# Kernel optimization log

Measured on AMD Instinct MI355X. Metric: run time of the kernel, lower is better.

## Reference

```python
import jax, jax.numpy as jnp
import numpy as np

N_QUBITS = 8
N_LAYERS = 3
N_FEATURES = 16
BATCH = 65536
DIM = 2 ** N_QUBITS  # 256 amplitudes
EPS = 1e-5  # torch BatchNorm1d default eps

# Precompute CNOT permutations (wire 0 = most significant bit, PennyLane order)
_idx = np.arange(DIM)
CNOT_PERMS = []
for _i in range(N_QUBITS):
    for _j in range(_i + 1, N_QUBITS):
        _c = (_idx >> (N_QUBITS - 1 - _i)) & 1
        CNOT_PERMS.append(np.where(_c == 1, _idx ^ (1 << (N_QUBITS - 1 - _j)), _idx))
# PauliZ sign table: (DIM, N_QUBITS), +1 for bit 0, -1 for bit 1
Z_SIGNS = np.stack([1.0 - 2.0 * ((_idx >> (N_QUBITS - 1 - i)) & 1) for i in range(N_QUBITS)], axis=1).astype(np.float32)


def _ry(theta):
    t = jnp.asarray(theta)
    c = jnp.cos(t / 2).astype(jnp.complex64)
    s = jnp.sin(t / 2).astype(jnp.complex64)
    return jnp.stack([jnp.stack([c, -s], -1), jnp.stack([s, c], -1)], -2)


def _rx(theta):
    t = jnp.asarray(theta)
    c = jnp.cos(t / 2).astype(jnp.complex64)
    s = (-1j) * jnp.sin(t / 2).astype(jnp.complex64)
    return jnp.stack([jnp.stack([c, s], -1), jnp.stack([s, c], -1)], -2)


def _rz(theta):
    e = jnp.exp(-0.5j * jnp.asarray(theta, jnp.complex64))
    z = jnp.zeros_like(e)
    return jnp.stack([jnp.stack([e, z], -1), jnp.stack([z, jnp.conj(e)], -1)], -2)


def _apply_1q(state, U, w):
    # state: (B, DIM); U: (2,2) shared or (B,2,2) per-sample; wire w
    B = state.shape[0]
    left, right = 2 ** w, 2 ** (N_QUBITS - 1 - w)
    s = state.reshape(B, left, 2, right)
    if U.ndim == 2:
        out = jnp.einsum('st,bpsq->bptq', U, s)
    else:
        out = jnp.einsum('bst,bpsq->bptq', U, s)
    return out.reshape(B, DIM)


def _quantum(angles, qw):
    # Batched state-vector simulation of the PennyLane circuit.
    # angles: (B, N_QUBITS) float32 encoding angles; qw: (N_LAYERS, N_QUBITS, 3)
    B = angles.shape[0]
    state = jnp.zeros((B, DIM), jnp.complex64).at[:, 0].set(1.0 + 0.0j)
    for i in range(N_QUBITS):  # RY(inputs[i]) encoding, per-sample angles
        state = _apply_1q(state, _ry(angles[:, i]), i)
    for l in range(N_LAYERS):
        for i in range(N_QUBITS):
            state = _apply_1q(state, _rx(qw[l, i, 0]), i)
            state = _apply_1q(state, _ry(qw[l, i, 1]), i)
            state = _apply_1q(state, _rz(qw[l, i, 2]), i)
        for perm in CNOT_PERMS:  # all-pairs CNOT(i, j), i < j
            state = state[:, perm]
    probs = state.real ** 2 + state.imag ** 2  # (B, DIM)
    return probs @ jnp.asarray(Z_SIGNS)  # (B, N_QUBITS) <Z_i> expectations


def _bn(h, g, b, m, v):
    # BatchNorm1d in inference mode (running stats)
    return (h - m) * jax.lax.rsqrt(v + EPS) * g + b


def _forward(x, W1, b1, g1, bt1, m1, v1, W2, b2, g2, bt2, m2, v2, W3, b3, q_weights, W4, b4, g4, bt4, m4, v4, W5, b5, W6, b6):
    h = jax.nn.relu(_bn(x @ W1.T + b1, g1, bt1, m1, v1))
    h = jax.nn.relu(_bn(h @ W2.T + b2, g2, bt2, m2, v2))
    pre = jnp.tanh(h @ W3.T + b3)  # (B, N_QUBITS)
    # Original detaches before the quantum circuit -> no grad through it
    q_out = _quantum(jax.lax.stop_gradient(pre), jax.lax.stop_gradient(q_weights))
    h = jax.nn.relu(_bn(q_out @ W4.T + b4, g4, bt4, m4, v4))
    h = jax.nn.relu(h @ W5.T + b5)
    return h @ W6.T + b6  # (B, 1)


def setup_inputs() -> dict:
    key = jax.random.key(0)
    ks = jax.random.split(key, 8)

    def lin(k, o, i):
        return (jax.random.normal(k, (o, i), jnp.float32) / np.sqrt(i)).astype(jnp.float32)

    return {
        'x': jax.random.normal(ks[0], (BATCH, N_FEATURES), jnp.float32),
        'W1': lin(ks[1], 128, N_FEATURES), 'b1': jnp.zeros((128,), jnp.float32),
        'g1': jnp.ones((128,), jnp.float32), 'bt1': jnp.zeros((128,), jnp.float32),
        'm1': jnp.zeros((128,), jnp.float32), 'v1': jnp.ones((128,), jnp.float32),
        'W2': lin(ks[2], 64, 128), 'b2': jnp.zeros((64,), jnp.float32),
        'g2': jnp.ones((64,), jnp.float32), 'bt2': jnp.zeros((64,), jnp.float32),
        'm2': jnp.zeros((64,), jnp.float32), 'v2': jnp.ones((64,), jnp.float32),
        'W3': lin(ks[3], N_QUBITS, 64), 'b3': jnp.zeros((N_QUBITS,), jnp.float32),
        'q_weights': jax.random.normal(ks[4], (N_LAYERS, N_QUBITS, 3), jnp.float32) * 0.1,
        'W4': lin(ks[5], 32, N_QUBITS), 'b4': jnp.zeros((32,), jnp.float32),
        'g4': jnp.ones((32,), jnp.float32), 'bt4': jnp.zeros((32,), jnp.float32),
        'm4': jnp.zeros((32,), jnp.float32), 'v4': jnp.ones((32,), jnp.float32),
        'W5': lin(ks[6], 16, 32), 'b5': jnp.zeros((16,), jnp.float32),
        'W6': lin(ks[7], 1, 16), 'b6': jnp.zeros((1,), jnp.float32),
    }


def reference(x, W1, b1, g1, bt1, m1, v1, W2, b2, g2, bt2, m2, v2, W3, b3, q_weights, W4, b4, g4, bt4, m4, v4, W5, b5, W6, b6):
    return _forward(x, W1, b1, g1, bt1, m1, v1, W2, b2, g2, bt2, m2, v2, W3, b3, q_weights, W4, b4, g4, bt4, m4, v4, W5, b5, W6, b6)
```

## Files before the change

### kernel.cpp

```cpp
#include <hip/hip_runtime.h>

__device__ __forceinline__ float2 cmul(float2 a, float2 b){
    return make_float2(a.x*b.x - a.y*b.y, a.x*b.y + a.y*b.x);
}
__device__ __forceinline__ float2 cadd(float2 a, float2 b){
    return make_float2(a.x + b.x, a.y + b.y);
}
__device__ __forceinline__ unsigned short f2h(float f){
    _Float16 h = (_Float16)f;
    return __builtin_bit_cast(unsigned short, h);
}

typedef _Float16 f16x8 __attribute__((ext_vector_type(8)));
typedef float    f32x4 __attribute__((ext_vector_type(4)));

__device__ __forceinline__ void split8(const float* p, f16x8& ah, f16x8& al){
    const f32x4* q = (const f32x4*)p;
    f32x4 v0 = q[0], v1 = q[1];
    float av[8] = {v0[0],v0[1],v0[2],v0[3],v1[0],v1[1],v1[2],v1[3]};
    #pragma unroll
    for (int j=0;j<8;++j){
        _Float16 h = (_Float16)av[j];
        ah[j] = h;
        al[j] = (_Float16)(av[j] - (float)h);
    }
}

__device__ __forceinline__ void build_gates(const float* qw, int l, int c, float2 (*G)[2][2]){
    if (c < 8){
        int i = c;
        float t0 = 0.5f*qw[l*24 + i*3 + 0];
        float t1 = 0.5f*qw[l*24 + i*3 + 1];
        float t2 = 0.5f*qw[l*24 + i*3 + 2];
        float c1,s1,c2,s2,c3,s3;
        sincosf(t0,&s1,&c1); sincosf(t1,&s2,&c2); sincosf(t2,&s3,&c3);
        float2 RX[2][2] = {{{c1,0.f},{0.f,-s1}},{{0.f,-s1},{c1,0.f}}};
        float2 RY[2][2] = {{{c2,0.f},{s2,0.f}},{{-s2,0.f},{c2,0.f}}};
        float2 M[2][2];
        #pragma unroll
        for (int r=0;r<2;++r)
            #pragma unroll
            for (int cc=0;cc<2;++cc)
                M[r][cc] = cadd(cmul(RY[r][0],RX[0][cc]), cmul(RY[r][1],RX[1][cc]));
        float2 e  = {c3,-s3};
        float2 ec = {c3, s3};
        G[i][0][0]=cmul(e, M[0][0]); G[i][0][1]=cmul(e, M[0][1]);
        G[i][1][0]=cmul(ec,M[1][0]); G[i][1][1]=cmul(ec,M[1][1]);
    }
}
__device__ __forceinline__ int cnot_perm(int k){
    int r = k;
    for (int i=6;i>=0;--i)
        for (int j=7;j>i;--j)
            if ((r >> (7-i)) & 1) r ^= 1 << (7-j);
    return r;
}

__global__ void k_prep(const float* __restrict__ W1, const float* __restrict__ b1,
                       const float* __restrict__ g1, const float* __restrict__ bt1,
                       const float* __restrict__ m1, const float* __restrict__ v1,
                       const float* __restrict__ W2, const float* __restrict__ b2,
                       const float* __restrict__ g2, const float* __restrict__ bt2,
                       const float* __restrict__ m2, const float* __restrict__ v2,
                       const float* __restrict__ W3,
                       unsigned short* __restrict__ H1w, float* __restrict__ c1,
                       unsigned short* __restrict__ H2w, float* __restrict__ c2,
                       unsigned short* __restrict__ H3w){
    int tid = blockIdx.x*256 + threadIdx.x;
    int stride = gridDim.x*256;
    for (int i=tid; i<4096; i+=stride){ int n=i>>5, k=i&31;
        float s=g1[n]*rsqrtf(v1[n]+1e-5f);
        H1w[i] = f2h(k<16 ? W1[n*16+k]*s : 0.f); }
    for (int i=tid; i<128;  i+=stride){ float s=g1[i]*rsqrtf(v1[i]+1e-5f); c1[i]=(b1[i]-m1[i])*s+bt1[i]; }
    for (int i=tid; i<8192; i+=stride){ int n=i>>7;
        float s=g2[n]*rsqrtf(v2[n]+1e-5f);
        H2w[i] = f2h(W2[i]*s); }
    for (int i=tid; i<64;   i+=stride){ float s=g2[i]*rsqrtf(v2[i]+1e-5f); c2[i]=(b2[i]-m2[i])*s+bt2[i]; }
    for (int i=tid; i<1024; i+=stride){ int n=i>>6, k=i&63;
        H3w[i] = f2h(n<8 ? W3[n*64+k] : 0.f); }
}

__global__ void k_build_layers(const float* __restrict__ qw, float2* __restrict__ U){
    __shared__ float2 G[8][2][2];
    int l = blockIdx.y, k = blockIdx.x, c = threadIdx.x;
    build_gates(qw, l, c, G);
    __syncthreads();
    int r = cnot_perm(k);
    float2 p = {1.f, 0.f};
    #pragma unroll
    for (int i=0;i<8;++i)
        p = cmul(p, G[i][(r>>(7-i))&1][(c>>(7-i))&1]);
    U[l*65536 + k*256 + c] = p;
}

__global__ __launch_bounds__(256) void k_rowmm(const float* __restrict__ qw,
                                              const float2* __restrict__ U,
                                              unsigned short* __restrict__ W){
    __shared__ float2 G[8][2][2];
    __shared__ float2 vs[256];
    __shared__ float2 ws[256];
    int r = blockIdx.x, c = threadIdx.x;
    build_gates(qw, 2, c, G);
    __syncthreads();
    int pr = cnot_perm(r);
    float2 p = {1.f, 0.f};
    #pragma unroll
    for (int i=0;i<8;++i)
        p = cmul(p, G[i][(pr>>(7-i))&1][(c>>(7-i))&1]);
    vs[c] = p;
    __syncthreads();
    float2 acc = {0.f,0.f};
    #pragma unroll 8
    for (int m=0;m<256;++m)
        acc = cadd(acc, cmul(vs[m], U[65536 + m*256 + c]));
    ws[c] = acc;
    __syncthreads();
    float2 z = {0.f,0.f};
    #pragma unroll 8
    for (int m=0;m<256;++m)
        z = cadd(z, cmul(ws[m], U[m*256 + c]));
    W[r*256 + c]       = f2h(z.x);
    W[(r+256)*256 + c] = f2h(z.y);
}

__global__ __launch_bounds__(256,2) void k_front(
    const float* __restrict__ x,
    const unsigned short* __restrict__ H1w, const float* __restrict__ c1,
    const unsigned short* __restrict__ H2w, const float* __restrict__ c2,
    const unsigned short* __restrict__ H3w, const float* __restrict__ b3,
    float* __restrict__ pre)
{
    __shared__ __align__(16) char smem[60416];
    float* XS = (float*)smem;
    float* H1 = (float*)(smem + 9216);
    float* H2 = (float*)(smem + 43008);

    int tid = threadIdx.x;
    int row0 = blockIdx.x*64;
    {
        int r = tid >> 2, q = tid & 3;
        const float4* xp = (const float4*)(x + (row0 + r)*16 + q*4);
        float4 v = xp[0];
        *(float4*)(XS + r*36 + q*4) = v;
        *(float4*)(XS + r*36 + 16 + q*4) = make_float4(0.f,0.f,0.f,0.f);
    }
    __syncthreads();

    int wave = tid>>6, lane = tid&63, l15 = lane&15, lq = lane>>4;
    const f32x4 zz = {0.f,0.f,0.f,0.f};

    f32x4 acc1[4][2];
    #pragma unroll
    for (int mt=0;mt<4;++mt){ acc1[mt][0]=zz; acc1[mt][1]=zz; }
    #pragma unroll
    for (int mt=0; mt<4; ++mt){
        f16x8 ah, al;
        split8(XS + (mt*16+l15)*36 + lq*8, ah, al);
        #pragma unroll
        for (int t=0;t<2;++t){
            int nt = wave + t*4;
            f16x8 b = *(const f16x8*)(H1w + (nt*16+l15)*32 + lq*8);
            acc1[mt][t] = __builtin_amdgcn_mfma_f32_16x16x32_f16(ah, b, acc1[mt][t], 0,0,0);
            acc1[mt][t] = __builtin_amdgcn_mfma_f32_16x16x32_f16(al, b, acc1[mt][t], 0,0,0);
        }
    }
    #pragma unroll
    for (int t=0;t<2;++t){
        int n = (wave + t*4)*16 + l15;
        float bias = c1[n];
        #pragma unroll
        for (int mt=0; mt<4; ++mt)
            #pragma unroll
            for (int reg=0; reg<4; ++reg){
                int rowl = mt*16 + lq*4 + reg;
                H1[rowl*132 + n] = fmaxf(acc1[mt][t][reg] + bias, 0.f);
            }
    }
    __syncthreads();

    f32x4 acc2[4];
    #pragma unroll
    for (int mt=0;mt<4;++mt) acc2[mt]=zz;
    #pragma unroll
    for (int ks=0; ks<4; ++ks){
        f16x8 b = *(const f16x8*)(H2w + (wave*16+l15)*128 + ks*32 + lq*8);
        #pragma unroll
        for (int mt=0; mt<4; ++mt){
            f16x8 ah, al;
            split8(H1 + (mt*16+l15)*132 + ks*32 + lq*8, ah, al);
            acc2[mt] = __builtin_amdgcn_mfma_f32_16x16x32_f16(ah, b, acc2[mt], 0,0,0);
            acc2[mt] = __builtin_amdgcn_mfma_f32_16x16x32_f16(al, b, acc2[mt], 0,0,0);
        }
    }
    {
        int n = wave*16 + l15;
        float bias = c2[n];
        #pragma unroll
        for (int mt=0; mt<4; ++mt)
            #pragma unroll
            for (int reg=0; reg<4; ++reg){
                int rowl = mt*16 + lq*4 + reg;
                H2[rowl*68 + n] = fmaxf(acc2[mt][reg] + bias, 0.f);
            }
    }
    __syncthreads();

    f32x4 acc3 = zz;
    #pragma unroll
    for (int ks=0; ks<2; ++ks){
        f16x8 b = *(const f16x8*)(H3w + l15*64 + ks*32 + lq*8);
        f16x8 ah, al;
        split8(H2 + (wave*16+l15)*68 + ks*32 + lq*8, ah, al);
        acc3 = __builtin_amdgcn_mfma_f32_16x16x32_f16(ah, b, acc3, 0,0,0);
        acc3 = __builtin_amdgcn_mfma_f32_16x16x32_f16(al, b, acc3, 0,0,0);
    }
    if (l15 < 8){
        float bias = b3[l15];
        #pragma unroll
        for (int reg=0; reg<4; ++reg){
            int rowl = wave*16 + lq*4 + reg;
            pre[(row0+rowl)*8 + l15] = tanhf(acc3[reg] + bias);
        }
    }
}

#define A_STRIDE 264
#define P_STRIDE 268
__global__ __launch_bounds__(256,2) void k_main(
    const float* __restrict__ pre, const unsigned short* __restrict__ Wq,
    const float* __restrict__ W4, const float* __restrict__ b4, const float* __restrict__ g4,
    const float* __restrict__ bt4, const float* __restrict__ m4, const float* __restrict__ v4,
    const float* __restrict__ W5, const float* __restrict__ b5,
    const float* __restrict__ W6, const float* __restrict__ b6,
    float* __restrict__ out)
{
    __shared__ __align__(16) char smem[34304 + 4096 + 2048];
    unsigned short* As = (unsigned short*)smem;
    float* probs = (float*)smem;
    float* qacc  = (float*)(smem + 34304);
    float* qout  = (float*)(smem + 34304 + 4096);

    int tid = threadIdx.x;
    {
        int row = tid & 63, q = tid >> 6;
        int grow = blockIdx.x*64 + row;
        const float4* p4 = (const float4*)(pre + grow*8);
        float4 pa = p4[0], pb = p4[1];
        float th[8] = {pa.x,pa.y,pa.z,pa.w,pb.x,pb.y,pb.z,pb.w};
        float cs[8], sn[8];
        #pragma unroll
        for (int i=0;i<8;++i){ __sincosf(0.5f*th[i], &sn[i], &cs[i]); sn[i] = -sn[i]; }
        float F = (q&2 ? sn[0] : cs[0]) * (q&1 ? sn[1] : cs[1]);
        float Pm[8], Pl[8];
        #pragma unroll
        for (int a2=0;a2<8;++a2){
            Pm[a2] = (a2&4?sn[2]:cs[2]) * (a2&2?sn[3]:cs[3]) * (a2&1?sn[4]:cs[4]);
            Pl[a2] = (a2&4?sn[5]:cs[5]) * (a2&2?sn[6]:cs[6]) * (a2&1?sn[7]:cs[7]);
        }
        unsigned short* arow = As + row*A_STRIDE + q*64;
        #pragma unroll
        for (int mh=0;mh<8;++mh){
            float fm = F * Pm[mh];
            uint4 w;
            w.x = (unsigned)f2h(fm*Pl[0]) | ((unsigned)f2h(fm*Pl[1])<<16);
            w.y = (unsigned)f2h(fm*Pl[2]) | ((unsigned)f2h(fm*Pl[3])<<16);
            w.z = (unsigned)f2h(fm*Pl[4]) | ((unsigned)f2h(fm*Pl[5])<<16);
            w.w = (unsigned)f2h(fm*Pl[6]) | ((unsigned)f2h(fm*Pl[7])<<16);
            *reinterpret_cast<uint4*>(arow + mh*8) = w;
        }
    }
    __syncthreads();

    int wave = tid >> 6, lane = tid & 63;
    int l15 = lane & 15, lq = lane >> 4;

    const f16x8* Bp[8];
    #pragma unroll
    for (int t=0;t<8;++t){
        int n = wave*64 + (t&3)*16 + ((t>>2)<<8) + l15;
        Bp[t] = reinterpret_cast<const f16x8*>(Wq + n*256 + lq*8);
    }
    const f16x8* Ap[4];
    #pragma unroll
    for (int mt=0;mt<4;++mt)
        Ap[mt] = reinterpret_cast<const f16x8*>(As + (mt*16 + l15)*A_STRIDE + lq*8);

    f32x4 acc[4][8];
    const f32x4 zz = {0.f,0.f,0.f,0.f};
    #pragma unroll
    for (int mt=0;mt<4;++mt)
        #pragma unroll
        for (int t=0;t<8;++t) acc[mt][t] = zz;

    f16x8 bfr[2][8];
    #pragma unroll
    for (int t=0;t<8;++t) bfr[0][t] = Bp[t][0];

    #pragma unroll
    for (int ks=0;ks<8;++ks){
        int cur = ks & 1;
        if (ks < 7){
            #pragma unroll
            for (int t=0;t<8;++t) bfr[cur^1][t] = Bp[t][(ks+1)*4];
        }
        f16x8 afr[4];
        #pragma unroll
        for (int mt=0;mt<4;++mt) afr[mt] = Ap[mt][ks*4];
        #pragma unroll
        for (int mt=0;mt<4;++mt)
            #pragma unroll
            for (int t=0;t<8;++t)
                acc[mt][t] = __builtin_amdgcn_mfma_f32_16x16x32_f16(afr[mt], bfr[cur][t], acc[mt][t], 0, 0, 0);
    }
    __syncthreads();

    #pragma unroll
    for (int h=0; h<2; ++h){
        #pragma unroll
        for (int mtl=0; mtl<2; ++mtl){
            int mt = h*2 + mtl;
            #pragma unroll
            for (int t=0;t<4;++t){
                #pragma unroll
                for (int reg=0;reg<4;++reg){
                    float sr = acc[mt][t][reg];
                    float si = acc[mt][t+4][reg];
                    int prow = mtl*16 + lq*4 + reg;
                    int pcol = wave*64 + t*16 + l15;
                    probs[prow*P_STRIDE + pcol] = fmaf(sr,sr,si*si);
                }
            }
        }
        __syncthreads();
        if (tid < 128){
            int row = tid & 31, kg = tid >> 5;
            const float* pb = probs + row*P_STRIDE + kg*64;
            float S=0.f,q2=0.f,q3=0.f,q4=0.f,q5=0.f,q6=0.f,q7=0.f;
            #pragma unroll
            for (int j=0;j<64;++j){
                float p = pb[j];
                S  += p;
                q2 += (j&32)? -p : p;
                q3 += (j&16)? -p : p;
                q4 += (j&8) ? -p : p;
                q5 += (j&4) ? -p : p;
                q6 += (j&2) ? -p : p;
                q7 += (j&1) ? -p : p;
            }
            float* qa = qacc + tid*8;
            qa[0] = (kg&2)? -S : S;
            qa[1] = (kg&1)? -S : S;
            qa[2]=q2; qa[3]=q3; qa[4]=q4; qa[5]=q5; qa[6]=q6; qa[7]=q7;
        }
        __syncthreads();
        {
            int r = tid >> 3, i = tid & 7;
            float v = qacc[r*8+i] + qacc[(32+r)*8+i] + qacc[(64+r)*8+i] + qacc[(96+r)*8+i];
            qout[(h*32 + r)*8 + i] = v;
        }
    }
    __syncthreads();

    if (tid < 64){
        int r = tid;
        float qv[8];
        #pragma unroll
        for (int i=0;i<8;++i) qv[i] = qout[r*8+i];
        float h4[32];
        #pragma unroll
        for (int j=0;j<32;++j){
            float a = b4[j];
            #pragma unroll
            for (int i=0;i<8;++i) a = fmaf(qv[i], W4[j*8+i], a);
            float sc = g4[j]*rsqrtf(v4[j]+1e-5f);
            a = fmaf(a - m4[j], sc, bt4[j]);
            h4[j] = fmaxf(a, 0.f);
        }
        float h5[16];
        #pragma unroll
        for (int j=0;j<16;++j){
            float a = b5[j];
            #pragma unroll
            for (int k=0;k<32;++k) a = fmaf(h4[k], W5[j*32+k], a);
            h5[j] = fmaxf(a, 0.f);
        }
        float o = b6[0];
        #pragma unroll
        for (int k=0;k<16;++k) o = fmaf(h5[k], W6[k], o);
        out[blockIdx.x*64 + r] = o;
    }
}

extern "C" void kernel_launch(void* const* d_in, const int* in_sizes, int n_in,
                              void* d_out, int out_size, void* d_ws, size_t ws_size,
                              hipStream_t stream) {
    (void)in_sizes; (void)n_in; (void)out_size; (void)ws_size;
    const float* x   = (const float*)d_in[0];
    const float* W1  = (const float*)d_in[1];
    const float* b1  = (const float*)d_in[2];
    const float* g1  = (const float*)d_in[3];
    const float* bt1 = (const float*)d_in[4];
    const float* m1  = (const float*)d_in[5];
    const float* v1  = (const float*)d_in[6];
    const float* W2  = (const float*)d_in[7];
    const float* b2  = (const float*)d_in[8];
    const float* g2  = (const float*)d_in[9];
    const float* bt2 = (const float*)d_in[10];
    const float* m2  = (const float*)d_in[11];
    const float* v2  = (const float*)d_in[12];
    const float* W3  = (const float*)d_in[13];
    const float* b3  = (const float*)d_in[14];
    const float* qw  = (const float*)d_in[15];
    const float* W4  = (const float*)d_in[16];
    const float* b4  = (const float*)d_in[17];
    const float* g4  = (const float*)d_in[18];
    const float* bt4 = (const float*)d_in[19];
    const float* m4  = (const float*)d_in[20];
    const float* v4  = (const float*)d_in[21];
    const float* W5  = (const float*)d_in[22];
    const float* b5  = (const float*)d_in[23];
    const float* W6  = (const float*)d_in[24];
    const float* b6  = (const float*)d_in[25];

    char* ws = (char*)d_ws;
    float2* U   = (float2*)ws;
    unsigned short* Wq = (unsigned short*)(U + 2*65536);
    float* pre  = (float*)(Wq + 512*256);
    unsigned short* H1w = (unsigned short*)(pre + 65536*8);
    unsigned short* H2w = H1w + 4096;
    unsigned short* H3w = H2w + 8192;
    float* c1 = (float*)(H3w + 1024);
    float* c2 = c1 + 128;

    k_prep<<<8, 256, 0, stream>>>(W1,b1,g1,bt1,m1,v1, W2,b2,g2,bt2,m2,v2, W3,
                                  H1w,c1,H2w,c2,H3w);
    k_build_layers<<<dim3(256,2), 256, 0, stream>>>(qw, U);
    k_rowmm<<<256, 256, 0, stream>>>(qw, U, Wq);
    k_front<<<1024, 256, 0, stream>>>(x, H1w,c1, H2w,c2, H3w,b3, pre);
    k_main<<<1024, 256, 0, stream>>>(pre, Wq, W4,b4,g4,bt4,m4,v4, W5,b5,W6,b6,
                                     (float*)d_out);
}
```

Before: 198.1 us.

## Fuse prep into layer-build kernel and store Wq in MFMA fragment order

Merges the weight-prep kernel into the layer-building kernel using an extra grid row, removing one launch. It also has the row-matmul kernel write the quantum transfer matrix pre-swizzled into MFMA B-fragment order. Each lane of k_main then loads its fragments as contiguous 16-byte chunks instead of strided rows, which should coalesce the B loads. The cost is a scattered write pattern in k_rowmm, which is a small kernel.

```diff
diff --git a/kernel.cpp b/kernel.cpp
--- a/kernel.cpp
+++ b/kernel.cpp
@@ -56,7 +56,8 @@
     return r;
 }
 
-__global__ void k_prep(const float* __restrict__ W1, const float* __restrict__ b1,
+__global__ void k_build_prep(const float* __restrict__ qw, float2* __restrict__ U,
+                       const float* __restrict__ W1, const float* __restrict__ b1,
                        const float* __restrict__ g1, const float* __restrict__ bt1,
                        const float* __restrict__ m1, const float* __restrict__ v1,
                        const float* __restrict__ W2, const float* __restrict__ b2,
@@ -66,21 +67,22 @@
                        unsigned short* __restrict__ H1w, float* __restrict__ c1,
                        unsigned short* __restrict__ H2w, float* __restrict__ c2,
                        unsigned short* __restrict__ H3w){
-    int tid = blockIdx.x*256 + threadIdx.x;
-    int stride = gridDim.x*256;
-    for (int i=tid; i<4096; i+=stride){ int n=i>>5, k=i&31;
-        float s=g1[n]*rsqrtf(v1[n]+1e-5f);
-        H1w[i] = f2h(k<16 ? W1[n*16+k]*s : 0.f); }
-    for (int i=tid; i<128;  i+=stride){ float s=g1[i]*rsqrtf(v1[i]+1e-5f); c1[i]=(b1[i]-m1[i])*s+bt1[i]; }
-    for (int i=tid; i<8192; i+=stride){ int n=i>>7;
-        float s=g2[n]*rsqrtf(v2[n]+1e-5f);
-        H2w[i] = f2h(W2[i]*s); }
-    for (int i=tid; i<64;   i+=stride){ float s=g2[i]*rsqrtf(v2[i]+1e-5f); c2[i]=(b2[i]-m2[i])*s+bt2[i]; }
-    for (int i=tid; i<1024; i+=stride){ int n=i>>6, k=i&63;
-        H3w[i] = f2h(n<8 ? W3[n*64+k] : 0.f); }
-}
-
-__global__ void k_build_layers(const float* __restrict__ qw, float2* __restrict__ U){
+    if (blockIdx.y == 2){
+        if (blockIdx.x >= 8) return;
+        int tid = blockIdx.x*256 + threadIdx.x;
+        const int stride = 8*256;
+        for (int i=tid; i<4096; i+=stride){ int n=i>>5, k=i&31;
+            float s=g1[n]*rsqrtf(v1[n]+1e-5f);
+            H1w[i] = f2h(k<16 ? W1[n*16+k]*s : 0.f); }
+        for (int i=tid; i<128;  i+=stride){ float s=g1[i]*rsqrtf(v1[i]+1e-5f); c1[i]=(b1[i]-m1[i])*s+bt1[i]; }
+        for (int i=tid; i<8192; i+=stride){ int n=i>>7;
+            float s=g2[n]*rsqrtf(v2[n]+1e-5f);
+            H2w[i] = f2h(W2[i]*s); }
+        for (int i=tid; i<64;   i+=stride){ float s=g2[i]*rsqrtf(v2[i]+1e-5f); c2[i]=(b2[i]-m2[i])*s+bt2[i]; }
+        for (int i=tid; i<1024; i+=stride){ int n=i>>6, k=i&63;
+            H3w[i] = f2h(n<8 ? W3[n*64+k] : 0.f); }
+        return;
+    }
     __shared__ float2 G[8][2][2];
     int l = blockIdx.y, k = blockIdx.x, c = threadIdx.x;
     build_gates(qw, l, c, G);
@@ -95,7 +97,7 @@
 
 __global__ __launch_bounds__(256) void k_rowmm(const float* __restrict__ qw,
                                               const float2* __restrict__ U,
-                                              unsigned short* __restrict__ W){
+                                              unsigned short* __restrict__ WqS){
     __shared__ float2 G[8][2][2];
     __shared__ float2 vs[256];
     __shared__ float2 ws[256];
@@ -119,8 +121,11 @@
     #pragma unroll 8
     for (int m=0;m<256;++m)
         z = cadd(z, cmul(ws[m], U[m*256 + c]));
-    W[r*256 + c]       = f2h(z.x);
-    W[(r+256)*256 + c] = f2h(z.y);
+    int T = r >> 4, l15 = r & 15;
+    int ks = c >> 5, lq = (c >> 3) & 3, j = c & 7;
+    int lane = lq*16 + l15;
+    WqS[((T     *8 + ks)*64 + lane)*8 + j] = f2h(z.x);
+    WqS[(((T+16)*8 + ks)*64 + lane)*8 + j] = f2h(z.y);
 }
 
 __global__ __launch_bounds__(256,2) void k_front(
@@ -227,7 +232,7 @@
 #define A_STRIDE 264
 #define P_STRIDE 268
 __global__ __launch_bounds__(256,2) void k_main(
-    const float* __restrict__ pre, const unsigned short* __restrict__ Wq,
+    const float* __restrict__ pre, const unsigned short* __restrict__ WqS,
     const float* __restrict__ W4, const float* __restrict__ b4, const float* __restrict__ g4,
     const float* __restrict__ bt4, const float* __restrict__ m4, const float* __restrict__ v4,
     const float* __restrict__ W5, const float* __restrict__ b5,
@@ -277,8 +282,8 @@
     const f16x8* Bp[8];
     #pragma unroll
     for (int t=0;t<8;++t){
-        int n = wave*64 + (t&3)*16 + ((t>>2)<<8) + l15;
-        Bp[t] = reinterpret_cast<const f16x8*>(Wq + n*256 + lq*8);
+        int T = ((t>>2)<<4) + wave*4 + (t&3);
+        Bp[t] = reinterpret_cast<const f16x8*>(WqS + T*4096) + lane;
     }
     const f16x8* Ap[4];
     #pragma unroll
@@ -301,7 +306,7 @@
         int cur = ks & 1;
         if (ks < 7){
             #pragma unroll
-            for (int t=0;t<8;++t) bfr[cur^1][t] = Bp[t][(ks+1)*4];
+            for (int t=0;t<8;++t) bfr[cur^1][t] = Bp[t][(ks+1)*64];
         }
         f16x8 afr[4];
         #pragma unroll
@@ -424,19 +429,19 @@
 
     char* ws = (char*)d_ws;
     float2* U   = (float2*)ws;
-    unsigned short* Wq = (unsigned short*)(U + 2*65536);
-    float* pre  = (float*)(Wq + 512*256);
+    unsigned short* WqS = (unsigned short*)(U + 2*65536);
+    float* pre  = (float*)(WqS + 512*256);
     unsigned short* H1w = (unsigned short*)(pre + 65536*8);
     unsigned short* H2w = H1w + 4096;
     unsigned short* H3w = H2w + 8192;
     float* c1 = (float*)(H3w + 1024);
     float* c2 = c1 + 128;
 
-    k_prep<<<8, 256, 0, stream>>>(W1,b1,g1,bt1,m1,v1, W2,b2,g2,bt2,m2,v2, W3,
+    k_build_prep<<<dim3(256,3), 256, 0, stream>>>(qw, U,
+                                  W1,b1,g1,bt1,m1,v1, W2,b2,g2,bt2,m2,v2, W3,
                                   H1w,c1,H2w,c2,H3w);
-    k_build_layers<<<dim3(256,2), 256, 0, stream>>>(qw, U);
-    k_rowmm<<<256, 256, 0, stream>>>(qw, U, Wq);
+    k_rowmm<<<256, 256, 0, stream>>>(qw, U, WqS);
     k_front<<<1024, 256, 0, stream>>>(x, H1w,c1, H2w,c2, H3w,b3, pre);
-    k_main<<<1024, 256, 0, stream>>>(pre, Wq, W4,b4,g4,bt4,m4,v4, W5,b5,W6,b6,
+    k_main<<<1024, 256, 0, stream>>>(pre, WqS, W4,b4,g4,bt4,m4,v4, W5,b5,W6,b6,
                                      (float*)d_out);
 }
```

After: 183.3 us. -7.5%, faster.
